# Performance work log

Measured on AMD Instinct MI355X. Metric: run time of the kernel, lower is better.

The kernel has to match this reference:

```python
import jax, jax.numpy as jnp
import numpy as np

B, S, H, L = 4, 2048, 1024, 4
CLAMP_LO, CLAMP_HI = 1e-8, 1.0 - 1e-8
LN_EPS = 1e-5


def setup_inputs() -> dict:
    key = jax.random.key(0)
    ks = jax.random.split(key, 13)
    s = 1.0 / np.sqrt(H)
    u = lambda k, shape: jax.random.uniform(k, shape, jnp.float32, -s, s)
    return {
        "x": jax.random.normal(ks[0], (B, S, H), jnp.float32),
        "fwd_Wz": u(ks[1], (L, H, H)), "fwd_bz": u(ks[2], (L, H)),
        "fwd_Wh": u(ks[3], (L, H, H)), "fwd_bh": u(ks[4], (L, H)),
        "bwd_Wz": u(ks[5], (L, H, H)), "bwd_bz": u(ks[6], (L, H)),
        "bwd_Wh": u(ks[7], (L, H, H)), "bwd_bh": u(ks[8], (L, H)),
        "fusion_W": u(ks[9], (H, 2 * H)), "fusion_b": u(ks[10], (H,)),
        "ln_gamma": jnp.ones((H,), jnp.float32),
        "ln_beta": jnp.zeros((H,), jnp.float32),
    }


def _linear_scan(a, b):
    # h_t = a_t * h_{t-1} + b_t over axis 1 (seq), via associative scan.
    # composition: (a2,b2) o (a1,b1) = (a2*a1, a2*b1 + b2)
    def combine(left, right):
        al, bl = left
        ar, br = right
        return (ar * al, ar * bl + br)
    _, h = jax.lax.associative_scan(combine, (a, b), axis=1)
    return h


def _mingru(x, Wz, bz, Wh, bh):
    # x: (B,S,H); Wz,Wh: (H_out,H_in) like nn.Linear
    z = jax.nn.sigmoid(jnp.einsum('bsi,hi->bsh', x, Wz) + bz)
    h_tilde = jnp.tanh(jnp.einsum('bsi,hi->bsh', x, Wh) + bh)
    a = jnp.clip(1.0 - z, CLAMP_LO, CLAMP_HI)
    return _linear_scan(a, z * h_tilde)


def _layernorm(x, gamma, beta):
    mu = jnp.mean(x, axis=-1, keepdims=True)
    var = jnp.mean(jnp.square(x - mu), axis=-1, keepdims=True)
    return (x - mu) * jax.lax.rsqrt(var + LN_EPS) * gamma + beta


def _stack(x, Wz, bz, Wh, bh, gamma, beta):
    h = x
    for i in range(L):
        h_new = _mingru(h, Wz[i], bz[i], Wh[i], bh[i])
        if i > 0:
            h_new = h_new + h  # residual (shapes match for i>0)
        h = _layernorm(h_new, gamma, beta)
    return h


def reference(x, fwd_Wz, fwd_bz, fwd_Wh, fwd_bh,
              bwd_Wz, bwd_bz, bwd_Wh, bwd_bh,
              fusion_W, fusion_b, ln_gamma, ln_beta):
    h_fwd = _stack(x, fwd_Wz, fwd_bz, fwd_Wh, fwd_bh, ln_gamma, ln_beta)
    h_bwd = _stack(jnp.flip(x, axis=1), bwd_Wz, bwd_bz, bwd_Wh, bwd_bh,
                   ln_gamma, ln_beta)
    h_bwd = jnp.flip(h_bwd, axis=1)
    h_comb = jnp.concatenate([h_fwd, h_bwd], axis=-1)  # (B,S,2H)
    return jnp.einsum('bsi,hi->bsh', h_comb, fusion_W) + fusion_b
```

## Files before the change

kernel.cpp:

```cpp
#include <hip/hip_runtime.h>
#include <stdint.h>

#define Bn 4
#define Sn 2048
#define Hn 1024
#define Ln 4
#define Mn (Bn*Sn)
#define CHUNK 32
#define NCH (Sn/CHUNK)

typedef __bf16 bf16x8 __attribute__((ext_vector_type(8)));
typedef float  f32x4  __attribute__((ext_vector_type(4)));
typedef uint32_t u32;

__device__ __forceinline__ unsigned short f2bf(float f) {
  uint32_t u = __float_as_uint(f);
  uint32_t r = (u + 0x7FFFu + ((u >> 16) & 1u)) >> 16;
  return (unsigned short)r;
}
__device__ __forceinline__ float bf2f(unsigned short u) {
  return __uint_as_float(((uint32_t)u) << 16);
}

__device__ __forceinline__ void gload_lds16(const void* g, void* l) {
  __builtin_amdgcn_global_load_lds((const __attribute__((address_space(1))) void*)g,
                                   (__attribute__((address_space(3))) void*)l, 16, 0, 0);
}

__global__ __launch_bounds__(256) void cast_all(
    const float* __restrict__ s0, const float* __restrict__ s1,
    const float* __restrict__ s2, const float* __restrict__ s3,
    const float* __restrict__ s4, const float* __restrict__ s5,
    unsigned short* __restrict__ d0, unsigned short* __restrict__ d1,
    unsigned short* __restrict__ d2, unsigned short* __restrict__ d3,
    unsigned short* __restrict__ d4, unsigned short* __restrict__ d5) {
  long i = (long)blockIdx.x * 256 + threadIdx.x;
  const float* s; unsigned short* d; long off;
  if      (i < 1048576) { s = s0; d = d0; off = i; }
  else if (i < 2097152) { s = s1; d = d1; off = i - 1048576; }
  else if (i < 3145728) { s = s2; d = d2; off = i - 2097152; }
  else if (i < 4194304) { s = s3; d = d3; off = i - 3145728; }
  else if (i < 4718592) { s = s4; d = d4; off = i - 4194304; }
  else                  { s = s5; d = d5; off = i - 4718592; }
  float4 v = reinterpret_cast<const float4*>(s)[off];
  ushort4 o;
  o.x = f2bf(v.x); o.y = f2bf(v.y); o.z = f2bf(v.z); o.w = f2bf(v.w);
  reinterpret_cast<ushort4*>(d)[off] = o;
}


#define DSR(d, b, imm) \
  asm volatile("ds_read_b128 %0, %1 offset:%c2" : "=&v"(d) : "v"(b), "i"(imm))

#define VMW(n) do { \
    asm volatile("s_waitcnt vmcnt(" #n ")"); \
    __builtin_amdgcn_sched_barrier(0); \
  } while (0)

#define LGKM(n) do { \
    asm volatile("s_waitcnt lgkmcnt(" #n ")"); \
    __builtin_amdgcn_sched_barrier(0); \
  } while (0)

#define DSR4(ARR, base, off) do { \
    DSR(ARR[0], base, (off)); \
    DSR(ARR[1], base, (off) + 1024); \
    DSR(ARR[2], base, (off) + 2048); \
    DSR(ARR[3], base, (off) + 3072); \
  } while (0)

#define CL(ARR, BARR, MB) do { \
    __builtin_amdgcn_s_setprio(1); \
    _Pragma("unroll") \
    for (int _m = 0; _m < 4; ++_m) { \
      _Pragma("unroll") \
      for (int _n = 0; _n < 4; ++_n) \
        acc[(MB) + _m][_n] = __builtin_amdgcn_mfma_f32_16x16x32_bf16( \
            ARR[_m], BARR[_n], acc[(MB) + _m][_n], 0, 0, 0); \
    } \
    __builtin_amdgcn_s_setprio(0); \
  } while (0)

#define BODY(buf) do { \
    if constexpr (MF == 8) { \
      DSR4(aA, baseA, ((buf) * 2 + 0) * RGA); \
      DSR4(b0, baseB, ((buf) * 2 + 0) * 16384); \
      DSR4(aB, baseA, ((buf) * 2 + 0) * RGA + 4096); \
      LGKM(4); \
      CL(aA, b0, 0); \
      DSR4(b1, baseB, ((buf) * 2 + 1) * 16384); \
      LGKM(4); \
      CL(aB, b0, 4); \
      DSR4(aA, baseA, ((buf) * 2 + 1) * RGA); \
      LGKM(4); \
      DSR4(aB, baseA, ((buf) * 2 + 1) * RGA + 4096); \
      LGKM(4); \
      CL(aA, b1, 0); \
      LGKM(0); \
      CL(aB, b1, 4); \
    } else { \
      DSR4(aA, baseA, ((buf) * 2 + 0) * RGA); \
      DSR4(b0, baseB, ((buf) * 2 + 0) * 16384); \
      DSR4(aB, baseA, ((buf) * 2 + 1) * RGA); \
      LGKM(4); \
      CL(aA, b0, 0); \
      DSR4(b1, baseB, ((buf) * 2 + 1) * 16384); \
      LGKM(0); \
      CL(aB, b1, 0); \
    } \
  } while (0)

template<int MF>
__global__ __launch_bounds__(512, 2) void gemm_t(
    const unsigned short* __restrict__ act,
    const unsigned short* __restrict__ Wlo,
    const unsigned short* __restrict__ Whi,
    const float* __restrict__ bias0, const float* __restrict__ bias1,
    int Nsplit, float* __restrict__ out, unsigned short* __restrict__ outbf,
    int Ndim, int K) {
  constexpr int BMR = MF * 32;
  constexpr int RGA = BMR * 64;
  __shared__ unsigned char smA[4 * RGA];
  __shared__ unsigned char smB[65536];
  const int tid  = threadIdx.x;
  const int lane = tid & 63;
  const int w    = tid >> 6;
  const int waveM = w >> 2;
  const int waveN = w & 3;
  const int bm = blockIdx.x, bn = blockIdx.y;

  const unsigned short* Wp; int nbase;
  if (bn * 256 < Nsplit) { Wp = Wlo; nbase = bn * 256; }
  else                   { Wp = Whi; nbase = bn * 256 - Nsplit; }

  const int swz  = (((lane >> 4) ^ ((lane >> 1) & 3)) << 4);
  const int aoff = (waveM * (MF * 16) + (lane & 15)) * 64 + swz;
  const int boff = (waveN * 64 + (lane & 15)) * 64 + swz;

  const u32 baseA = (u32)(size_t)(void*)&smA[0] + (u32)aoff;
  const u32 baseB = (u32)(size_t)(void*)&smB[0] + (u32)boff;

  const int srow = tid >> 2;
  const int slog = (tid & 3) ^ ((srow >> 1) & 3);
  const unsigned short* aS0 = act + (size_t)(bm * BMR + srow) * K + slog * 8;
  const unsigned short* aS1 = aS0 + (size_t)128 * K;
  const unsigned short* bS0 = Wp  + (size_t)(nbase + srow) * K + slog * 8;
  const unsigned short* bS1 = bS0 + (size_t)128 * K;
  const int wB = w * 1024;

  f32x4 acc[MF][4];
#pragma unroll
  for (int m = 0; m < MF; ++m)
#pragma unroll
    for (int n = 0; n < 4; ++n) acc[m][n] = (f32x4)0.0f;

  bf16x8 aA[4], aB[4], b0[4], b1[4];

  auto STG4 = [&](int t, int buf) {
#pragma unroll
    for (int kh = 0; kh < 2; ++kh) {
      unsigned char* ra = smA + (buf * 2 + kh) * RGA;
      gload_lds16(aS0 + (size_t)t * 64 + kh * 32, ra + wB);
      if constexpr (MF == 8)
        gload_lds16(aS1 + (size_t)t * 64 + kh * 32, ra + 8192 + wB);
      unsigned char* rb = smB + (buf * 2 + kh) * 16384;
      gload_lds16(bS0 + (size_t)t * 64 + kh * 32, rb + wB);
      gload_lds16(bS1 + (size_t)t * 64 + kh * 32, rb + 8192 + wB);
    }
  };

  const int nkt   = K >> 6;
  const int niter = nkt >> 1;

  STG4(0, 0);
  VMW(0);
  __builtin_amdgcn_s_barrier();

  for (int j = 0; j < niter - 1; ++j) {
    STG4(2 * j + 1, 1); BODY(0); VMW(0); __builtin_amdgcn_s_barrier();
    STG4(2 * j + 2, 0); BODY(1); VMW(0); __builtin_amdgcn_s_barrier();
  }
  STG4(nkt - 1, 1); BODY(0); VMW(0); __builtin_amdgcn_s_barrier();
  BODY(1);

  const int colBase = bn * 256 + waveN * 64;
  const int rowBase = bm * BMR + waveM * (MF * 16);
#pragma unroll
  for (int m = 0; m < MF; ++m) {
#pragma unroll
    for (int n = 0; n < 4; ++n) {
      int col = colBase + n * 16 + (lane & 15);
      float bv = (col < Nsplit) ? bias0[col] : bias1[col - Nsplit];
      if (outbf) {
#pragma unroll
        for (int r = 0; r < 4; ++r) {
          int row = rowBase + m * 16 + (lane >> 4) * 4 + r;
          outbf[(size_t)row * Ndim + col] = f2bf(acc[m][n][r] + bv);
        }
      } else {
#pragma unroll
        for (int r = 0; r < 4; ++r) {
          int row = rowBase + m * 16 + (lane >> 4) * 4 + r;
          out[(size_t)row * Ndim + col] = acc[m][n][r] + bv;
        }
      }
    }
  }
}

__device__ __forceinline__ void gate_ab(float zp, float hp, float& a, float& bv) {
  float z  = 1.0f / (1.0f + __expf(-zp));
  float e  = __expf(-2.0f * fabsf(hp));
  float th = (1.0f - e) / (1.0f + e);
  th = (hp >= 0.0f) ? th : -th;
  a  = fminf(fmaxf(1.0f - z, 1e-8f), 1.0f - 1e-8f);
  bv = z * th;
}

__global__ __launch_bounds__(256) void scan_p1(const unsigned short* __restrict__ pre,
                                               float* __restrict__ Ac, float* __restrict__ Bc,
                                               int dir) {
  int tid = threadIdx.x;
  int bid = blockIdx.x;
  int ht = bid & 3;
  int c  = (bid >> 2) & (NCH - 1);
  int b  = bid >> 8;
  int h  = ht * 256 + tid;
  float Aa = 1.0f, Bb = 0.0f;
  for (int j = 0; j < CHUNK; ++j) {
    int t = c * CHUNK + j;
    int s = dir ? (Sn - 1 - t) : t;
    const unsigned short* p = pre + (size_t)(b * Sn + s) * 2048;
    float a, bv;
    gate_ab(bf2f(p[h]), bf2f(p[1024 + h]), a, bv);
    Aa = a * Aa;
    Bb = a * Bb + bv;
  }
  Ac[(size_t)(b * NCH + c) * Hn + h] = Aa;
  Bc[(size_t)(b * NCH + c) * Hn + h] = Bb;
}

__global__ __launch_bounds__(1024) void scan_p3_ln(
    const unsigned short* __restrict__ pre,
    const float* __restrict__ Ac, const float* __restrict__ Bc,
    const unsigned short* __restrict__ resid,
    const float* __restrict__ gamma, const float* __restrict__ beta,
    unsigned short* __restrict__ out_bf,
    int bf_stride, int bf_off, int dir) {
  __shared__ unsigned short hsl[CHUNK][Hn];
  const int h = threadIdx.x;
  const int c = blockIdx.x & (NCH - 1);
  const int b = blockIdx.x >> 6;

  float hprev = 0.0f;
  {
    int cc = 0;
    for (; cc + 8 <= c; cc += 8) {
      float Af[8], Bf[8];
#pragma unroll
      for (int q = 0; q < 8; ++q) {
        size_t idx = (size_t)(b * NCH + cc + q) * Hn + h;
        Af[q] = Ac[idx];
        Bf[q] = Bc[idx];
      }
#pragma unroll
      for (int q = 0; q < 8; ++q) hprev = Af[q] * hprev + Bf[q];
    }
    for (; cc < c; ++cc) {
      size_t idx = (size_t)(b * NCH + cc) * Hn + h;
      hprev = Ac[idx] * hprev + Bc[idx];
    }
  }

  for (int j = 0; j < CHUNK; ++j) {
    int t = c * CHUNK + j;
    int s = dir ? (Sn - 1 - t) : t;
    const unsigned short* p = pre + (size_t)(b * Sn + s) * 2048;
    float a, bv;
    gate_ab(bf2f(p[h]), bf2f(p[1024 + h]), a, bv);
    hprev = a * hprev + bv;
    hsl[j][h] = f2bf(hprev);
  }
  __syncthreads();

  const int lane = h & 63;
  const int wv   = h >> 6;
  float gm[16], bt[16];
  {
    const float4* gp = reinterpret_cast<const float4*>(gamma);
    const float4* bp = reinterpret_cast<const float4*>(beta);
#pragma unroll
    for (int half = 0; half < 2; ++half) {
      int base = half * 128 + lane * 2;
#pragma unroll
      for (int i = 0; i < 2; ++i) {
        float4 g4 = gp[base + i], b4 = bp[base + i];
        int o = half * 8 + i * 4;
        gm[o+0] = g4.x; gm[o+1] = g4.y; gm[o+2] = g4.z; gm[o+3] = g4.w;
        bt[o+0] = b4.x; bt[o+1] = b4.y; bt[o+2] = b4.z; bt[o+3] = b4.w;
      }
    }
  }

  for (int rr = 0; rr < 2; ++rr) {
    const int j = wv * 2 + rr;
    const int t = c * CHUNK + j;
    const int s = dir ? (Sn - 1 - t) : t;
    const size_t row = (size_t)(b * Sn + s);

    const uint4* rp = reinterpret_cast<const uint4*>(&hsl[j][0]);
    uint4 q0 = rp[lane], q1 = rp[64 + lane];
    uint32_t uw[8] = {q0.x, q0.y, q0.z, q0.w, q1.x, q1.y, q1.z, q1.w};
    float v[16];
#pragma unroll
    for (int k = 0; k < 8; ++k) {
      v[2*k]   = bf2f((unsigned short)(uw[k] & 0xffffu));
      v[2*k+1] = bf2f((unsigned short)(uw[k] >> 16));
    }
    if (resid) {
      const uint4* rf = reinterpret_cast<const uint4*>(resid + row * Hn);
      uint4 r0v = rf[lane], r1v = rf[64 + lane];
      uint32_t rw[8] = {r0v.x, r0v.y, r0v.z, r0v.w, r1v.x, r1v.y, r1v.z, r1v.w};
#pragma unroll
      for (int k = 0; k < 8; ++k) {
        v[2*k]   += bf2f((unsigned short)(rw[k] & 0xffffu));
        v[2*k+1] += bf2f((unsigned short)(rw[k] >> 16));
      }
    }
    float s1 = 0.0f, s2 = 0.0f;
#pragma unroll
    for (int m = 0; m < 16; ++m) { s1 += v[m]; s2 += v[m] * v[m]; }
#pragma unroll
    for (int off = 1; off < 64; off <<= 1) {
      s1 += __shfl_xor(s1, off);
      s2 += __shfl_xor(s2, off);
    }
    float mu  = s1 * (1.0f / Hn);
    float var = s2 * (1.0f / Hn) - mu * mu;
    float rs  = rsqrtf(var + 1e-5f);

    float o[16];
#pragma unroll
    for (int m = 0; m < 16; ++m) o[m] = (v[m] - mu) * rs * gm[m] + bt[m];

    uint4* ob = reinterpret_cast<uint4*>(out_bf + row * bf_stride + bf_off);
    uint4 w0, w1;
    w0.x = f2bf(o[0])  | ((u32)f2bf(o[1])  << 16);
    w0.y = f2bf(o[2])  | ((u32)f2bf(o[3])  << 16);
    w0.z = f2bf(o[4])  | ((u32)f2bf(o[5])  << 16);
    w0.w = f2bf(o[6])  | ((u32)f2bf(o[7])  << 16);
    w1.x = f2bf(o[8])  | ((u32)f2bf(o[9])  << 16);
    w1.y = f2bf(o[10]) | ((u32)f2bf(o[11]) << 16);
    w1.z = f2bf(o[12]) | ((u32)f2bf(o[13]) << 16);
    w1.w = f2bf(o[14]) | ((u32)f2bf(o[15]) << 16);
    ob[lane]      = w0;
    ob[64 + lane] = w1;
  }
}

extern "C" void kernel_launch(void* const* d_in, const int* in_sizes, int n_in,
                              void* d_out, int out_size, void* d_ws, size_t ws_size,
                              hipStream_t stream) {
  const float* x        = (const float*)d_in[0];
  const float* fwd_Wz   = (const float*)d_in[1];
  const float* fwd_bz   = (const float*)d_in[2];
  const float* fwd_Wh   = (const float*)d_in[3];
  const float* fwd_bh   = (const float*)d_in[4];
  const float* bwd_Wz   = (const float*)d_in[5];
  const float* bwd_bz   = (const float*)d_in[6];
  const float* bwd_Wh   = (const float*)d_in[7];
  const float* bwd_bh   = (const float*)d_in[8];
  const float* fusion_W = (const float*)d_in[9];
  const float* fusion_b = (const float*)d_in[10];
  const float* gamma    = (const float*)d_in[11];
  const float* beta     = (const float*)d_in[12];
  float* out = (float*)d_out;

  unsigned short* WzA    = (unsigned short*)d_ws;
  unsigned short* WhA    = WzA + 8ULL * 1024 * 1024;
  unsigned short* fusWbf = WhA + 8ULL * 1024 * 1024;
  unsigned short* xbf    = fusWbf + 2ULL * 1024 * 1024;
  unsigned short* actbf  = xbf + 8ULL * 1024 * 1024;
  unsigned short* combbf = actbf + 8ULL * 1024 * 1024;
  float* actf = (float*)(combbf + 16ULL * 1024 * 1024);
  float* pre  = actf + 8ULL * 1024 * 1024;
  float* hs   = pre + 16ULL * 1024 * 1024;
  float* Ac   = hs + 8ULL * 1024 * 1024;
  float* Bc   = Ac + (size_t)Bn * NCH * Hn;
  float* pref = Bc + (size_t)Bn * NCH * Hn;
  size_t need = (size_t)((char*)(pref + (size_t)Bn * NCH * Hn) - (char*)d_ws);
  if (ws_size < need) return;
  unsigned short* prebf = (unsigned short*)pre;

  cast_all<<<26624, 256, 0, stream>>>(
      fwd_Wz, bwd_Wz, fwd_Wh, bwd_Wh, fusion_W, x,
      WzA, WzA + 4ULL * 1024 * 1024, WhA, WhA + 4ULL * 1024 * 1024, fusWbf, xbf);

  for (int d = 0; d < 2; ++d) {
    const float* bz = d ? bwd_bz : fwd_bz;
    const float* bh = d ? bwd_bh : fwd_bh;
    for (int l = 0; l < Ln; ++l) {
      const unsigned short* a_in = (l == 0) ? xbf : actbf;
      const unsigned short* Wlo = WzA + (size_t)(d * 4 + l) * 1024 * 1024;
      const unsigned short* Whi = WhA + (size_t)(d * 4 + l) * 1024 * 1024;
      gemm_t<8><<<dim3(Mn / 256, 2048 / 256), 512, 0, stream>>>(
          a_in, Wlo, Whi, bz + l * 1024, bh + l * 1024, 1024,
          nullptr, prebf, 2048, 1024);
      scan_p1<<<Bn * NCH * 4, 256, 0, stream>>>(prebf, Ac, Bc, d);
      if (l < Ln - 1)
        scan_p3_ln<<<Bn * NCH, 1024, 0, stream>>>(
            prebf, Ac, Bc, (l == 0) ? nullptr : actbf, gamma, beta,
            actbf, 1024, 0, d);
      else
        scan_p3_ln<<<Bn * NCH, 1024, 0, stream>>>(
            prebf, Ac, Bc, actbf, gamma, beta,
            combbf, 2048, d * 1024, d);
    }
  }
  gemm_t<4><<<dim3(Mn / 128, 1024 / 256), 512, 0, stream>>>(
      combbf, fusWbf, fusWbf, fusion_b, fusion_b, 1 << 30, out, nullptr, 1024, 2048);
}
```

Baseline: 681.0 us.

## Fuse minGRU gate computation into the projection GEMM epilogue

The Wz/Wh projection GEMM now loads matching 128-column tiles of both weight matrices per block, so each wave holds z and h pre-activations for the same columns. The epilogue computes sigmoid, tanh, clamp and z*h̃ and writes the scan coefficients a and b in bf16. The two scan kernels then read a and b directly and no longer evaluate the transcendentals twice per element. This removes the repeated gate math in both scan passes at the cost of a heavier GEMM epilogue. It also rounds a to bf16, where before only the pre-activations were rounded, which may change accuracy.

```diff
diff --git a/kernel.cpp b/kernel.cpp
--- a/kernel.cpp
+++ b/kernel.cpp
@@ -25,6 +25,15 @@
 __device__ __forceinline__ void gload_lds16(const void* g, void* l) {
   __builtin_amdgcn_global_load_lds((const __attribute__((address_space(1))) void*)g,
                                    (__attribute__((address_space(3))) void*)l, 16, 0, 0);
+}
+
+__device__ __forceinline__ void gate_ab(float zp, float hp, float& a, float& bv) {
+  float z  = 1.0f / (1.0f + __expf(-zp));
+  float e  = __expf(-2.0f * fabsf(hp));
+  float th = (1.0f - e) / (1.0f + e);
+  th = (hp >= 0.0f) ? th : -th;
+  a  = fminf(fmaxf(1.0f - z, 1e-8f), 1.0f - 1e-8f);
+  bv = z * th;
 }
 
 __global__ __launch_bounds__(256) void cast_all(
@@ -62,11 +71,18 @@
     __builtin_amdgcn_sched_barrier(0); \
   } while (0)
 
-#define DSR4(ARR, base, off) do { \
-    DSR(ARR[0], base, (off)); \
-    DSR(ARR[1], base, (off) + 1024); \
-    DSR(ARR[2], base, (off) + 2048); \
-    DSR(ARR[3], base, (off) + 3072); \
+#define DSRA4(ARR, off) do { \
+    DSR(ARR[0], baseA, (off)); \
+    DSR(ARR[1], baseA, (off) + 1024); \
+    DSR(ARR[2], baseA, (off) + 2048); \
+    DSR(ARR[3], baseA, (off) + 3072); \
+  } while (0)
+
+#define DSRB4(ARR, off) do { \
+    DSR(ARR[0], baseB, (off)); \
+    DSR(ARR[1], baseB, (off) + 1024); \
+    DSR(ARR[2], baseB, (off) + OB2); \
+    DSR(ARR[3], baseB, (off) + OB3); \
   } while (0)
 
 #define CL(ARR, BARR, MB) do { \
@@ -83,34 +99,34 @@
 
 #define BODY(buf) do { \
     if constexpr (MF == 8) { \
-      DSR4(aA, baseA, ((buf) * 2 + 0) * RGA); \
-      DSR4(b0, baseB, ((buf) * 2 + 0) * 16384); \
-      DSR4(aB, baseA, ((buf) * 2 + 0) * RGA + 4096); \
+      DSRA4(aA, ((buf) * 2 + 0) * RGA); \
+      DSRB4(b0, ((buf) * 2 + 0) * 16384); \
+      DSRA4(aB, ((buf) * 2 + 0) * RGA + 4096); \
       LGKM(4); \
       CL(aA, b0, 0); \
-      DSR4(b1, baseB, ((buf) * 2 + 1) * 16384); \
+      DSRB4(b1, ((buf) * 2 + 1) * 16384); \
       LGKM(4); \
       CL(aB, b0, 4); \
-      DSR4(aA, baseA, ((buf) * 2 + 1) * RGA); \
+      DSRA4(aA, ((buf) * 2 + 1) * RGA); \
       LGKM(4); \
-      DSR4(aB, baseA, ((buf) * 2 + 1) * RGA + 4096); \
+      DSRA4(aB, ((buf) * 2 + 1) * RGA + 4096); \
       LGKM(4); \
       CL(aA, b1, 0); \
       LGKM(0); \
       CL(aB, b1, 4); \
     } else { \
-      DSR4(aA, baseA, ((buf) * 2 + 0) * RGA); \
-      DSR4(b0, baseB, ((buf) * 2 + 0) * 16384); \
-      DSR4(aB, baseA, ((buf) * 2 + 1) * RGA); \
+      DSRA4(aA, ((buf) * 2 + 0) * RGA); \
+      DSRB4(b0, ((buf) * 2 + 0) * 16384); \
+      DSRA4(aB, ((buf) * 2 + 1) * RGA); \
       LGKM(4); \
       CL(aA, b0, 0); \
-      DSR4(b1, baseB, ((buf) * 2 + 1) * 16384); \
+      DSRB4(b1, ((buf) * 2 + 1) * 16384); \
       LGKM(0); \
       CL(aB, b1, 0); \
     } \
   } while (0)
 
-template<int MF>
+template<int MF, bool GATE>
 __global__ __launch_bounds__(512, 2) void gemm_t(
     const unsigned short* __restrict__ act,
     const unsigned short* __restrict__ Wlo,
@@ -120,6 +136,8 @@
     int Ndim, int K) {
   constexpr int BMR = MF * 32;
   constexpr int RGA = BMR * 64;
+  constexpr int OB2 = GATE ? 8192 : 2048;
+  constexpr int OB3 = GATE ? 9216 : 3072;
   __shared__ unsigned char smA[4 * RGA];
   __shared__ unsigned char smB[65536];
   const int tid  = threadIdx.x;
@@ -129,13 +147,9 @@
   const int waveN = w & 3;
   const int bm = blockIdx.x, bn = blockIdx.y;
 
-  const unsigned short* Wp; int nbase;
-  if (bn * 256 < Nsplit) { Wp = Wlo; nbase = bn * 256; }
-  else                   { Wp = Whi; nbase = bn * 256 - Nsplit; }
-
   const int swz  = (((lane >> 4) ^ ((lane >> 1) & 3)) << 4);
   const int aoff = (waveM * (MF * 16) + (lane & 15)) * 64 + swz;
-  const int boff = (waveN * 64 + (lane & 15)) * 64 + swz;
+  const int boff = ((GATE ? waveN * 32 : waveN * 64) + (lane & 15)) * 64 + swz;
 
   const u32 baseA = (u32)(size_t)(void*)&smA[0] + (u32)aoff;
   const u32 baseB = (u32)(size_t)(void*)&smB[0] + (u32)boff;
@@ -144,8 +158,17 @@
   const int slog = (tid & 3) ^ ((srow >> 1) & 3);
   const unsigned short* aS0 = act + (size_t)(bm * BMR + srow) * K + slog * 8;
   const unsigned short* aS1 = aS0 + (size_t)128 * K;
-  const unsigned short* bS0 = Wp  + (size_t)(nbase + srow) * K + slog * 8;
-  const unsigned short* bS1 = bS0 + (size_t)128 * K;
+  const unsigned short *bS0, *bS1;
+  if constexpr (GATE) {
+    bS0 = Wlo + (size_t)(bn * 128 + srow) * K + slog * 8;
+    bS1 = Whi + (size_t)(bn * 128 + srow) * K + slog * 8;
+  } else {
+    const unsigned short* Wp; int nbase;
+    if (bn * 256 < Nsplit) { Wp = Wlo; nbase = bn * 256; }
+    else                   { Wp = Whi; nbase = bn * 256 - Nsplit; }
+    bS0 = Wp + (size_t)(nbase + srow) * K + slog * 8;
+    bS1 = bS0 + (size_t)128 * K;
+  }
   const int wB = w * 1024;
 
   f32x4 acc[MF][4];
@@ -183,38 +206,49 @@
   STG4(nkt - 1, 1); BODY(0); VMW(0); __builtin_amdgcn_s_barrier();
   BODY(1);
 
-  const int colBase = bn * 256 + waveN * 64;
   const int rowBase = bm * BMR + waveM * (MF * 16);
-#pragma unroll
-  for (int m = 0; m < MF; ++m) {
-#pragma unroll
-    for (int n = 0; n < 4; ++n) {
-      int col = colBase + n * 16 + (lane & 15);
-      float bv = (col < Nsplit) ? bias0[col] : bias1[col - Nsplit];
-      if (outbf) {
+  if constexpr (GATE) {
+#pragma unroll
+    for (int n = 0; n < 2; ++n) {
+      const int col = bn * 128 + waveN * 32 + n * 16 + (lane & 15);
+      const float bz = bias0[col];
+      const float bh = bias1[col];
+#pragma unroll
+      for (int m = 0; m < MF; ++m) {
 #pragma unroll
         for (int r = 0; r < 4; ++r) {
           int row = rowBase + m * 16 + (lane >> 4) * 4 + r;
-          outbf[(size_t)row * Ndim + col] = f2bf(acc[m][n][r] + bv);
-        }
-      } else {
-#pragma unroll
-        for (int r = 0; r < 4; ++r) {
-          int row = rowBase + m * 16 + (lane >> 4) * 4 + r;
-          out[(size_t)row * Ndim + col] = acc[m][n][r] + bv;
+          float a, bv;
+          gate_ab(acc[m][n][r] + bz, acc[m][n + 2][r] + bh, a, bv);
+          outbf[(size_t)row * 2048 + col]        = f2bf(a);
+          outbf[(size_t)row * 2048 + 1024 + col] = f2bf(bv);
         }
       }
     }
-  }
-}
-
-__device__ __forceinline__ void gate_ab(float zp, float hp, float& a, float& bv) {
-  float z  = 1.0f / (1.0f + __expf(-zp));
-  float e  = __expf(-2.0f * fabsf(hp));
-  float th = (1.0f - e) / (1.0f + e);
-  th = (hp >= 0.0f) ? th : -th;
-  a  = fminf(fmaxf(1.0f - z, 1e-8f), 1.0f - 1e-8f);
-  bv = z * th;
+  } else {
+    const int colBase = bn * 256 + waveN * 64;
+#pragma unroll
+    for (int m = 0; m < MF; ++m) {
+#pragma unroll
+      for (int n = 0; n < 4; ++n) {
+        int col = colBase + n * 16 + (lane & 15);
+        float bv = (col < Nsplit) ? bias0[col] : bias1[col - Nsplit];
+        if (outbf) {
+#pragma unroll
+          for (int r = 0; r < 4; ++r) {
+            int row = rowBase + m * 16 + (lane >> 4) * 4 + r;
+            outbf[(size_t)row * Ndim + col] = f2bf(acc[m][n][r] + bv);
+          }
+        } else {
+#pragma unroll
+          for (int r = 0; r < 4; ++r) {
+            int row = rowBase + m * 16 + (lane >> 4) * 4 + r;
+            out[(size_t)row * Ndim + col] = acc[m][n][r] + bv;
+          }
+        }
+      }
+    }
+  }
 }
 
 __global__ __launch_bounds__(256) void scan_p1(const unsigned short* __restrict__ pre,
@@ -231,8 +265,8 @@
     int t = c * CHUNK + j;
     int s = dir ? (Sn - 1 - t) : t;
     const unsigned short* p = pre + (size_t)(b * Sn + s) * 2048;
-    float a, bv;
-    gate_ab(bf2f(p[h]), bf2f(p[1024 + h]), a, bv);
+    float a  = bf2f(p[h]);
+    float bv = bf2f(p[1024 + h]);
     Aa = a * Aa;
     Bb = a * Bb + bv;
   }
@@ -276,8 +310,8 @@
     int t = c * CHUNK + j;
     int s = dir ? (Sn - 1 - t) : t;
     const unsigned short* p = pre + (size_t)(b * Sn + s) * 2048;
-    float a, bv;
-    gate_ab(bf2f(p[h]), bf2f(p[1024 + h]), a, bv);
+    float a  = bf2f(p[h]);
+    float bv = bf2f(p[1024 + h]);
     hprev = a * hprev + bv;
     hsl[j][h] = f2bf(hprev);
   }
@@ -403,7 +437,7 @@
       const unsigned short* a_in = (l == 0) ? xbf : actbf;
       const unsigned short* Wlo = WzA + (size_t)(d * 4 + l) * 1024 * 1024;
       const unsigned short* Whi = WhA + (size_t)(d * 4 + l) * 1024 * 1024;
-      gemm_t<8><<<dim3(Mn / 256, 2048 / 256), 512, 0, stream>>>(
+      gemm_t<8, true><<<dim3(Mn / 256, 8), 512, 0, stream>>>(
           a_in, Wlo, Whi, bz + l * 1024, bh + l * 1024, 1024,
           nullptr, prebf, 2048, 1024);
       scan_p1<<<Bn * NCH * 4, 256, 0, stream>>>(prebf, Ac, Bc, d);
@@ -417,6 +451,6 @@
             combbf, 2048, d * 1024, d);
     }
   }
-  gemm_t<4><<<dim3(Mn / 128, 1024 / 256), 512, 0, stream>>>(
+  gemm_t<4, false><<<dim3(Mn / 128, 1024 / 256), 512, 0, stream>>>(
       combbf, fusWbf, fusWbf, fusion_b, fusion_b, 1 << 30, out, nullptr, 1024, 2048);
 }
```

New measurement: 599.0 us. -12.0%, faster.
